# Kernel tuning notes

Measured on AMD Instinct MI355X. Metric: run time of the kernel, lower is better.

The kernel has to match this reference:

```python
import jax, jax.numpy as jnp
import numpy as np

D_MODEL = 1024
N_LAYER = 8
VOCAB = 32000
D_INNER = 2048
D_STATE = 16
DT_RANK = 64  # ceil(d_model/16)
KCONV = 4
SEQ = 2048


def causal_depthwise_conv(u, w):
    # u: [l, d_inner], w: [d_inner, 1, K]; causal padding (K-1, 0), groups=d_inner
    x = u.T[None]  # [1, d_inner, l]
    y = jax.lax.conv_general_dilated(
        x, w, window_strides=(1,), padding=[(KCONV - 1, 0)],
        dimension_numbers=("NCH", "OIH", "NCH"), feature_group_count=u.shape[1])
    return y[0].T  # [l, d_inner]


def selective_scan(u, dt, A, B, C, Dp):
    # u,dt: [l,d_in]; A: [d_in,n]; B,C: [l,n]; D: [d_in]; bilinear discretization
    dt_A = dt[:, :, None] * A[None, :, :]          # [l, d_in, n]
    dt_B = dt[:, :, None] * B[:, None, :]          # [l, d_in, n]
    denom = 1.0 - dt_A / 2
    dA = (1.0 + dt_A / 2) / denom
    dB = dt_B / denom

    def step(h, inp):
        ui, dAi, dBi, Ci = inp
        h = dAi * h + dBi * ui[:, None]            # [d_in, n]
        return h, h @ Ci                           # y_i: [d_in]

    h0 = jnp.zeros((u.shape[1], A.shape[1]), dtype=u.dtype)
    _, y = jax.lax.scan(step, h0, (u, dA, dB, C))
    return y + u * Dp


def mamba_layer(x, Wres, Win, Wconv, WB, WC, Wdt1, Wdt2, bdt, logA, Dp, Wout):
    # RMS pre-norm (no learned scale)
    xn = x * jax.lax.rsqrt(jnp.mean(x * x, axis=-1, keepdims=True) + 1e-6)
    res = xn @ Wres.T                              # [l, d_inner]
    u = xn @ Win.T                                 # [l, d_inner]
    u = causal_depthwise_conv(u, Wconv)
    u = jax.nn.silu(u)
    A = -jnp.exp(logA)                             # [d_inner, n]
    B = u @ WB.T                                   # [l, n]
    C = u @ WC.T                                   # [l, n]
    dt = jax.nn.softplus((u @ Wdt1.T) @ Wdt2.T + bdt)
    y = selective_scan(u, dt, A, B, C, Dp)
    y = y * jax.nn.silu(res)
    return x + y @ Wout.T                          # residual


def setup_inputs() -> dict:
    key = jax.random.key(0)
    ks = jax.random.split(key, 12)
    L = N_LAYER
    token_ids = jax.random.randint(ks[0], (SEQ,), 0, VOCAB)
    embed = jax.random.normal(ks[1], (VOCAB, D_MODEL), jnp.float32) * 0.02
    Wres = jax.random.normal(ks[2], (L, D_INNER, D_MODEL), jnp.float32) * 0.02
    Win = jax.random.normal(ks[3], (L, D_INNER, D_MODEL), jnp.float32) * 0.02
    Wconv = jax.random.normal(ks[4], (L, D_INNER, 1, KCONV), jnp.float32) * 0.3
    WB = jax.random.normal(ks[5], (L, D_STATE, D_INNER), jnp.float32) * 0.02
    WC = jax.random.normal(ks[6], (L, D_STATE, D_INNER), jnp.float32) * 0.02
    Wdt1 = jax.random.normal(ks[7], (L, DT_RANK, D_INNER), jnp.float32) / np.sqrt(D_INNER)
    Wdt2 = jax.random.uniform(ks[8], (L, D_INNER, DT_RANK), jnp.float32,
                              minval=-1 / np.sqrt(DT_RANK), maxval=1 / np.sqrt(DT_RANK))
    # inverse-softplus of dt ~ U[1e-3, 1e-1] in log space
    dt0 = jnp.exp(jax.random.uniform(ks[9], (L, D_INNER)) * (np.log(0.1) - np.log(0.001)) + np.log(0.001))
    bdt = dt0 + jnp.log(-jnp.expm1(-dt0))
    logA = jnp.log(jnp.broadcast_to(jnp.arange(1, D_STATE + 1, dtype=jnp.float32),
                                    (L, D_INNER, D_STATE)))
    Dp = jnp.ones((L, D_INNER), jnp.float32)
    Wout = jax.random.normal(ks[10], (L, D_MODEL, D_INNER), jnp.float32) * 0.02
    return dict(token_ids=token_ids, embed=embed, Wres=Wres, Win=Win, Wconv=Wconv,
                WB=WB, WC=WC, Wdt1=Wdt1, Wdt2=Wdt2, bdt=bdt, logA=logA, Dp=Dp, Wout=Wout)


def reference(token_ids, embed, Wres, Win, Wconv, WB, WC, Wdt1, Wdt2, bdt, logA, Dp, Wout):
    x = embed[token_ids]  # [l, d_model]
    for i in range(Wres.shape[0]):
        x = mamba_layer(x, Wres[i], Win[i], Wconv[i], WB[i], WC[i],
                        Wdt1[i], Wdt2[i], bdt[i], logA[i], Dp[i], Wout[i])
    return x @ embed.T  # [l, vocab] logits (tied embedding)
```

## Files before the change

kernel.cpp:

```cpp
#include <hip/hip_runtime.h>

#define SEQ 2048
#define DMODEL 1024
#define DINNER 2048
#define DSTATE 16
#define DTRANK 64
#define NLAYER 8
#define VOCAB 32000
#define NCHUNK 32
#define CLEN 64
#define PROJ_NCH 16
#define PROJ_KC 128

typedef float f32x4 __attribute__((ext_vector_type(4)));
typedef short bf16x8 __attribute__((ext_vector_type(8)));

__device__ __forceinline__ ushort f2bf(float f) {
  union { float f; unsigned u; } v; v.f = f;
  unsigned r = v.u + 0x7fffu + ((v.u >> 16) & 1u);
  return (ushort)(r >> 16);
}

__device__ __forceinline__ void lds_load16(const void* g, void* l) {
  __builtin_amdgcn_global_load_lds(
      (const __attribute__((address_space(1))) void*)g,
      (__attribute__((address_space(3))) void*)l, 16, 0, 0);
}

template<int BM, bool NTS>
__global__ __launch_bounds__(512, 2) void gemm8p_bt_bf16(
    const ushort* __restrict__ A, const ushort* __restrict__ B,
    float* __restrict__ C, int N, int K)
{
  constexpr int MFR = BM / 32;
  constexpr int MPP = MFR / 4;
  constexpr int ALOADS = BM / 128;
  __shared__ __align__(16) ushort As[2 * BM * 64];
  __shared__ __align__(16) ushort Bs[2 * 256 * 64];
  const int tid = threadIdx.x;
  const int lane = tid & 63;
  const int wid = tid >> 6;
  const int wr = wid >> 2, wc = wid & 3;
  const int rr = lane & 15, kq = lane >> 4;

  unsigned nwg = gridDim.x * gridDim.y;
  unsigned lb = blockIdx.y * gridDim.x + blockIdx.x;
  if ((nwg & 7u) == 0u) { unsigned cpx = nwg >> 3; lb = (lb & 7u) * cpx + (lb >> 3); }
  const int bm = (int)(lb % gridDim.x) * BM;
  const int bn = (int)(lb / gridDim.x) * 256;

  const ushort* Abase = A + (size_t)bm * K;
  const ushort* Bbase = B + (size_t)bn * K;

  auto stageA = [&](int buf, int h, int kt) {
    constexpr int HR = BM / 2;
#pragma unroll
    for (int L = 0; L < ALOADS; ++L) {
      int f = L * 512 + tid;
      int rl = f >> 3, g = f & 7;
      int gg = g ^ (rl & 7);
      lds_load16(Abase + (size_t)(h * HR + rl) * K + kt * 64 + gg * 8,
                 (void*)(As + buf * (BM * 64) + (h * HR + rl) * 64 + g * 8));
    }
  };
  auto stageB = [&](int buf, int h, int kt) {
#pragma unroll
    for (int L = 0; L < 2; ++L) {
      int f = L * 512 + tid;
      int rl = f >> 3, g = f & 7;
      int gg = g ^ (rl & 7);
      lds_load16(Bbase + (size_t)(h * 128 + rl) * K + kt * 64 + gg * 8,
                 (void*)(Bs + buf * (256 * 64) + (h * 128 + rl) * 64 + g * 8));
    }
  };
  auto rdA = [&](int buf, int r, int kbyte) {
    int sw = kbyte ^ ((r & 7) << 4);
    return *(const bf16x8*)(As + buf * (BM * 64) + r * 64 + (sw >> 1));
  };
  auto rdB = [&](int buf, int r, int kbyte) {
    int sw = kbyte ^ ((r & 7) << 4);
    return *(const bf16x8*)(Bs + buf * (256 * 64) + r * 64 + (sw >> 1));
  };

  f32x4 acc[MFR][4];
#pragma unroll
  for (int m = 0; m < MFR; ++m)
#pragma unroll
    for (int n = 0; n < 4; ++n) acc[m][n] = (f32x4){0.f, 0.f, 0.f, 0.f};

  const int NT = K >> 6;
  stageA(0, 0, 0); stageA(0, 1, 0); stageB(0, 0, 0); stageB(0, 1, 0);

  for (int t = 0; t < NT; ++t) {
    const int cur = t & 1;
    const bool more = (t + 1 < NT);
    if (more) stageA(cur ^ 1, 0, t + 1);
    if (more) {
      if constexpr (BM == 256) asm volatile("s_waitcnt vmcnt(2)" ::: "memory");
      else                     asm volatile("s_waitcnt vmcnt(1)" ::: "memory");
    } else {
      asm volatile("s_waitcnt vmcnt(0)" ::: "memory");
    }
    __syncthreads();

    bf16x8 bfr[4][2];
#pragma unroll
    for (int n = 0; n < 4; ++n)
#pragma unroll
      for (int kk = 0; kk < 2; ++kk)
        bfr[n][kk] = rdB(cur, wc * 64 + n * 16 + rr, kk * 64 + kq * 16);

#pragma unroll
    for (int mq = 0; mq < 4; ++mq) {
      if (mq == 1 && more) stageA(cur ^ 1, 1, t + 1);
      if (mq == 2 && more) stageB(cur ^ 1, 0, t + 1);
      if (mq == 3 && more) stageB(cur ^ 1, 1, t + 1);
      bf16x8 af[MPP][2];
#pragma unroll
      for (int mf = 0; mf < MPP; ++mf)
#pragma unroll
        for (int kk = 0; kk < 2; ++kk)
          af[mf][kk] = rdA(cur, wr * (BM / 2) + (mq * MPP + mf) * 16 + rr, kk * 64 + kq * 16);
      __builtin_amdgcn_s_setprio(1);
#pragma unroll
      for (int kk = 0; kk < 2; ++kk)
#pragma unroll
        for (int mf = 0; mf < MPP; ++mf)
#pragma unroll
          for (int n = 0; n < 4; ++n)
            acc[mq * MPP + mf][n] = __builtin_amdgcn_mfma_f32_16x16x32_bf16(
                af[mf][kk], bfr[n][kk], acc[mq * MPP + mf][n], 0, 0, 0);
      __builtin_amdgcn_s_setprio(0);
    }
    __syncthreads();
  }

  float* ep = (float*)Bs + wid * (16 * 68);
  const int cg = bn + wc * 64;
#pragma unroll
  for (int m = 0; m < MFR; ++m) {
    const int r0g = bm + wr * (BM / 2) + m * 16;
#pragma unroll
    for (int n = 0; n < 4; ++n)
#pragma unroll
      for (int j = 0; j < 4; ++j)
        ep[(kq * 4 + j) * 68 + n * 16 + rr] = acc[m][n][j];
#pragma unroll
    for (int i = 0; i < 4; ++i) {
      int row = i * 4 + kq;
      f32x4 v = *(const f32x4*)&ep[row * 68 + rr * 4];
      f32x4* dst = (f32x4*)&C[(size_t)(r0g + row) * N + cg + rr * 4];
      if constexpr (NTS) __builtin_nontemporal_store(v, dst);
      else *dst = v;
    }
  }
}

__global__ __launch_bounds__(256) void gemm_btk_bf16(
    const ushort* __restrict__ A, const ushort* __restrict__ B,
    float* __restrict__ Cp, int M, int N, int K)
{
  __shared__ __align__(16) ushort As[128 * 64];
  __shared__ __align__(16) ushort Bs[128 * 64];
  const int tid = threadIdx.x;
  const int lane = tid & 63;
  const int wave = tid >> 6;
  const int wr = wave >> 1, wc = wave & 1;
  const int KC = K >> 1;
  const int k0 = blockIdx.z * KC;

  unsigned nwg = gridDim.x * gridDim.y;
  unsigned lb = blockIdx.y * gridDim.x + blockIdx.x;
  if ((nwg & 7u) == 0u) {
    unsigned cpx = nwg >> 3;
    lb = (lb & 7u) * cpx + (lb >> 3);
  }
  const int bm = (lb % gridDim.x) * 128;
  const int bn = (lb / gridDim.x) * 128;
  const int rr = lane & 15, kq = lane >> 4;

  f32x4 acc[4][4];
#pragma unroll
  for (int m = 0; m < 4; ++m)
#pragma unroll
    for (int n = 0; n < 4; ++n) acc[m][n] = (f32x4){0.f, 0.f, 0.f, 0.f};

  for (int kt = 0; kt < KC; kt += 64) {
#pragma unroll
    for (int i = 0; i < 4; ++i) {
      int fb = i * 256 + tid;
      int row = fb >> 3, cb = fb & 7;
      lds_load16(A + (size_t)(bm + row) * K + k0 + kt + cb * 8, (void*)(As + (size_t)fb * 8));
      lds_load16(B + (size_t)(bn + row) * K + k0 + kt + cb * 8, (void*)(Bs + (size_t)fb * 8));
    }
    __syncthreads();
#pragma unroll
    for (int ks = 0; ks < 2; ++ks) {
      bf16x8 af[4], bfr[4];
      const int koff = ks * 32 + kq * 8;
#pragma unroll
      for (int m = 0; m < 4; ++m)
        af[m] = *(const bf16x8*)&As[(wr * 64 + m * 16 + rr) * 64 + koff];
#pragma unroll
      for (int n = 0; n < 4; ++n)
        bfr[n] = *(const bf16x8*)&Bs[(wc * 64 + n * 16 + rr) * 64 + koff];
#pragma unroll
      for (int m = 0; m < 4; ++m)
#pragma unroll
        for (int n = 0; n < 4; ++n)
          acc[m][n] = __builtin_amdgcn_mfma_f32_16x16x32_bf16(af[m], bfr[n], acc[m][n], 0, 0, 0);
    }
    __syncthreads();
  }
  float* C = Cp + (size_t)blockIdx.z * M * N;
#pragma unroll
  for (int m = 0; m < 4; ++m) {
    const int r0 = bm + wr * 64 + m * 16 + kq * 4;
#pragma unroll
    for (int n = 0; n < 4; ++n) {
      const int cc = bn + wc * 64 + n * 16 + rr;
#pragma unroll
      for (int j = 0; j < 4; ++j)
        C[(size_t)(r0 + j) * N + cc] = acc[m][n][j];
    }
  }
}

__global__ __launch_bounds__(256) void add3_kernel(
    const float* __restrict__ P0, const float* __restrict__ P1, float* __restrict__ x)
{
  size_t i = (size_t)blockIdx.x * 256 + threadIdx.x;
  float4 a = ((const float4*)P0)[i];
  float4 b = ((const float4*)P1)[i];
  float4 c = ((float4*)x)[i];
  c.x += a.x + b.x; c.y += a.y + b.y; c.z += a.z + b.z; c.w += a.w + b.w;
  ((float4*)x)[i] = c;
}

__global__ __launch_bounds__(256) void projgemm_f32(
    const float* __restrict__ A, const float* __restrict__ W,
    float* __restrict__ Cp, int M)
{
  __shared__ float As[64][65];
  __shared__ float Ws[96][65];
  const int t = threadIdx.x;
  const int bm = blockIdx.x * 64;
  const int kc = blockIdx.y * PROJ_KC;
  const int ty = t >> 4, tx = t & 15;
  const int r0 = ty * 4, c0 = tx * 6;
  float acc[4][6] = {};
  for (int kt = 0; kt < PROJ_KC; kt += 64) {
#pragma unroll
    for (int i = 0; i < 4; ++i) {
      int e4 = i * 256 + t;
      int r = e4 >> 4, c4 = (e4 & 15) * 4;
      *(float4*)&As[r][c4] = *(const float4*)&A[(size_t)(bm + r) * DINNER + kc + kt + c4];
    }
#pragma unroll
    for (int i = 0; i < 6; ++i) {
      int e4 = i * 256 + t;
      int r = e4 >> 4, c4 = (e4 & 15) * 4;
      *(float4*)&Ws[r][c4] = *(const float4*)&W[(size_t)r * DINNER + kc + kt + c4];
    }
    __syncthreads();
#pragma unroll 4
    for (int kk = 0; kk < 64; ++kk) {
      float a0 = As[r0][kk], a1 = As[r0 + 1][kk], a2 = As[r0 + 2][kk], a3 = As[r0 + 3][kk];
      float w0 = Ws[c0][kk], w1 = Ws[c0 + 1][kk], w2 = Ws[c0 + 2][kk];
      float w3 = Ws[c0 + 3][kk], w4 = Ws[c0 + 4][kk], w5 = Ws[c0 + 5][kk];
      acc[0][0] += a0 * w0; acc[0][1] += a0 * w1; acc[0][2] += a0 * w2;
      acc[0][3] += a0 * w3; acc[0][4] += a0 * w4; acc[0][5] += a0 * w5;
      acc[1][0] += a1 * w0; acc[1][1] += a1 * w1; acc[1][2] += a1 * w2;
      acc[1][3] += a1 * w3; acc[1][4] += a1 * w4; acc[1][5] += a1 * w5;
      acc[2][0] += a2 * w0; acc[2][1] += a2 * w1; acc[2][2] += a2 * w2;
      acc[2][3] += a2 * w3; acc[2][4] += a2 * w4; acc[2][5] += a2 * w5;
      acc[3][0] += a3 * w0; acc[3][1] += a3 * w1; acc[3][2] += a3 * w2;
      acc[3][3] += a3 * w3; acc[3][4] += a3 * w4; acc[3][5] += a3 * w5;
    }
    __syncthreads();
  }
  float* cp = Cp + (size_t)blockIdx.y * M * 96;
#pragma unroll
  for (int i = 0; i < 4; ++i)
#pragma unroll
    for (int j = 0; j < 6; ++j)
      cp[(size_t)(bm + r0 + i) * 96 + c0 + j] = acc[i][j];
}

__global__ __launch_bounds__(256) void proj_reduce(
    const float* __restrict__ Cp, float* __restrict__ bcdt, int M)
{
  int idx = blockIdx.x * 256 + threadIdx.x;
  float s = 0.f;
#pragma unroll
  for (int c = 0; c < PROJ_NCH; ++c) s += Cp[(size_t)c * M * 96 + idx];
  bcdt[idx] = s;
}

__global__ __launch_bounds__(256) void smallgemm_f32(
    const float* __restrict__ A, int lda,
    const float* __restrict__ W, int ldw,
    float* __restrict__ C, int ldc,
    const float* __restrict__ bias,
    int M, int N, int K, int act)
{
  __shared__ float As[64][65];
  __shared__ float Ws[64][65];
  const int t = threadIdx.x;
  const int bm = blockIdx.x * 64, bn = blockIdx.y * 64;
  const int r0 = (t >> 4) * 4;
  const int c0 = (t & 15) * 4;
  float acc[4][4] = {};

  for (int kt = 0; kt < K; kt += 64) {
#pragma unroll
    for (int i = 0; i < 16; ++i) {
      int idx = i * 256 + t;
      int r = idx >> 6, c = idx & 63;
      As[r][c] = A[(size_t)(bm + r) * lda + kt + c];
      int wrow = bn + r;
      Ws[r][c] = (wrow < N) ? W[(size_t)wrow * ldw + kt + c] : 0.f;
    }
    __syncthreads();
#pragma unroll 8
    for (int kk = 0; kk < 64; ++kk) {
      float a0 = As[r0][kk], a1 = As[r0 + 1][kk], a2 = As[r0 + 2][kk], a3 = As[r0 + 3][kk];
      float w0 = Ws[c0][kk], w1 = Ws[c0 + 1][kk], w2 = Ws[c0 + 2][kk], w3 = Ws[c0 + 3][kk];
      acc[0][0] += a0 * w0; acc[0][1] += a0 * w1; acc[0][2] += a0 * w2; acc[0][3] += a0 * w3;
      acc[1][0] += a1 * w0; acc[1][1] += a1 * w1; acc[1][2] += a1 * w2; acc[1][3] += a1 * w3;
      acc[2][0] += a2 * w0; acc[2][1] += a2 * w1; acc[2][2] += a2 * w2; acc[2][3] += a2 * w3;
      acc[3][0] += a3 * w0; acc[3][1] += a3 * w1; acc[3][2] += a3 * w2; acc[3][3] += a3 * w3;
    }
    __syncthreads();
  }
#pragma unroll
  for (int i = 0; i < 4; ++i)
#pragma unroll
    for (int j = 0; j < 4; ++j) {
      int cc = bn + c0 + j;
      if (cc < N) {
        float v = acc[i][j];
        if (bias) v += bias[cc];
        if (act == 1) v = (v > 20.f) ? v : log1pf(expf(v));
        C[(size_t)(bm + r0 + i) * ldc + cc] = v;
      }
    }
}

__global__ __launch_bounds__(256) void gather_kernel(
    const int* __restrict__ ids, const float* __restrict__ embed, float* __restrict__ x)
{
  int row = blockIdx.x;
  int id = ids[row];
  ((float4*)x)[(size_t)row * (DMODEL / 4) + threadIdx.x] =
      ((const float4*)(embed + (size_t)id * DMODEL))[threadIdx.x];
}

__global__ __launch_bounds__(256) void rmsnorm_kernel(
    const float* __restrict__ x, ushort* __restrict__ xnb)
{
  int row = blockIdx.x;
  float4 v = ((const float4*)(x + (size_t)row * DMODEL))[threadIdx.x];
  float s = v.x * v.x + v.y * v.y + v.z * v.z + v.w * v.w;
#pragma unroll
  for (int o = 32; o > 0; o >>= 1) s += __shfl_down(s, o);
  __shared__ float ws[4];
  if ((threadIdx.x & 63) == 0) ws[threadIdx.x >> 6] = s;
  __syncthreads();
  float tot = ws[0] + ws[1] + ws[2] + ws[3];
  float sc = rsqrtf(tot * (1.0f / DMODEL) + 1e-6f);
  ushort4 o4 = {f2bf(v.x * sc), f2bf(v.y * sc), f2bf(v.z * sc), f2bf(v.w * sc)};
  ((ushort4*)xnb)[(size_t)row * (DMODEL / 4) + threadIdx.x] = o4;
}

__global__ __launch_bounds__(256) void conv_silu_kernel(
    const float* __restrict__ u0, int ld, const float* __restrict__ Wconv,
    float* __restrict__ u)
{
  int idx = blockIdx.x * 256 + threadIdx.x;
  int d4 = idx & (DINNER / 4 - 1);
  int l = idx >> 9;
  int d0 = d4 * 4;
  float wt[4][4];
#pragma unroll
  for (int j = 0; j < 4; ++j) {
    float4 tv = *(const float4*)&Wconv[(d0 + j) * 4];
    wt[j][0] = tv.x; wt[j][1] = tv.y; wt[j][2] = tv.z; wt[j][3] = tv.w;
  }
  float a[4] = {0.f, 0.f, 0.f, 0.f};
#pragma unroll
  for (int k = 0; k < 4; ++k) {
    int ls = l - 3 + k;
    if (ls >= 0) {
      float4 uv = *(const float4*)&u0[(size_t)ls * ld + d0];
      a[0] += uv.x * wt[0][k];
      a[1] += uv.y * wt[1][k];
      a[2] += uv.z * wt[2][k];
      a[3] += uv.w * wt[3][k];
    }
  }
  float4 r;
  r.x = a[0] / (1.f + expf(-a[0]));
  r.y = a[1] / (1.f + expf(-a[1]));
  r.z = a[2] / (1.f + expf(-a[2]));
  r.w = a[3] / (1.f + expf(-a[3]));
  *(float4*)&u[(size_t)l * DINNER + d0] = r;
}

__global__ __launch_bounds__(256) void scan_pass1(
    const float* __restrict__ dt, const float* __restrict__ u,
    const float* __restrict__ bcdt, const float* __restrict__ logA,
    float* __restrict__ P, float* __restrict__ S)
{
  const int tid = threadIdx.x;
  const int n = tid & 15, dl = tid >> 4;
  const int dbase = blockIdx.x * 16;
  const int c = blockIdx.y;
  const int t0 = c * CLEN;
  const int d = dbase + dl;
  const float Aval = -expf(logA[d * DSTATE + n]);
  __shared__ float sdt[CLEN][16], su[CLEN][16], sB[CLEN][16];
  {
    int tt = tid >> 2, j0 = (tid & 3) * 4;
    *(float4*)&sdt[tt][j0] = *(const float4*)&dt[(size_t)(t0 + tt) * DINNER + dbase + j0];
    *(float4*)&su[tt][j0]  = *(const float4*)&u[(size_t)(t0 + tt) * DINNER + dbase + j0];
    *(float4*)&sB[tt][j0]  = *(const float4*)&bcdt[(size_t)(t0 + tt) * 96 + j0];
  }
  __syncthreads();
  float h = 0.f, pr = 1.f;
#pragma unroll 8
  for (int i = 0; i < CLEN; ++i) {
    float dtv = sdt[i][dl], uv = su[i][dl], Bv = sB[i][n];
    float dtA = dtv * Aval;
    float rinv = __builtin_amdgcn_rcpf(1.f - 0.5f * dtA);
    float dA = (1.f + 0.5f * dtA) * rinv;
    float dBu = dtv * Bv * rinv * uv;
    h = dA * h + dBu;
    pr *= dA;
  }
  size_t idx = (size_t)c * (DINNER * DSTATE) + (size_t)d * DSTATE + n;
  P[idx] = pr;
  S[idx] = h;
}

__global__ __launch_bounds__(256) void scan_pass2(
    const float* __restrict__ dt, const float* __restrict__ u,
    const float* __restrict__ bcdt, const float* __restrict__ logA,
    const float* __restrict__ Dp, const float* __restrict__ P,
    const float* __restrict__ S, const float* __restrict__ resu0,
    ushort* __restrict__ y2b)
{
  const int tid = threadIdx.x;
  const int n = tid & 15, dl = tid >> 4;
  const int dbase = blockIdx.x * 16;
  const int c = blockIdx.y;
  const int t0 = c * CLEN;
  const int d = dbase + dl;
  const float Aval = -expf(logA[d * DSTATE + n]);
  const float Dpv = Dp[d];
  __shared__ float sdt[CLEN][16], su[CLEN][16], sB[CLEN][16], sC[CLEN][16], sres[CLEN][16];
  {
    int tt = tid >> 2, j0 = (tid & 3) * 4;
    *(float4*)&sdt[tt][j0]  = *(const float4*)&dt[(size_t)(t0 + tt) * DINNER + dbase + j0];
    *(float4*)&su[tt][j0]   = *(const float4*)&u[(size_t)(t0 + tt) * DINNER + dbase + j0];
    *(float4*)&sB[tt][j0]   = *(const float4*)&bcdt[(size_t)(t0 + tt) * 96 + j0];
    *(float4*)&sC[tt][j0]   = *(const float4*)&bcdt[(size_t)(t0 + tt) * 96 + 16 + j0];
    *(float4*)&sres[tt][j0] = *(const float4*)&resu0[(size_t)(t0 + tt) * (2 * DINNER) + dbase + j0];
  }
  float h = 0.f;
  {
    const size_t base = (size_t)d * DSTATE + n;
#pragma unroll 4
    for (int cc = 0; cc < c; ++cc) {
      size_t o = (size_t)cc * (DINNER * DSTATE) + base;
      h = P[o] * h + S[o];
    }
  }
  __syncthreads();
#pragma unroll 4
  for (int i = 0; i < CLEN; ++i) {
    float dtv = sdt[i][dl], uv = su[i][dl];
    float dtA = dtv * Aval;
    float rinv = __builtin_amdgcn_rcpf(1.f - 0.5f * dtA);
    float dA = (1.f + 0.5f * dtA) * rinv;
    float dBu = dtv * sB[i][n] * rinv * uv;
    h = dA * h + dBu;
    float p = h * sC[i][n];
    p += __shfl_xor(p, 1);
    p += __shfl_xor(p, 2);
    p += __shfl_xor(p, 4);
    p += __shfl_xor(p, 8);
    if (n == 0) {
      float rv = sres[i][dl];
      float yv = (p + uv * Dpv) * (rv / (1.f + expf(-rv)));
      y2b[(size_t)(t0 + i) * DINNER + d] = f2bf(yv);
    }
  }
}

__global__ __launch_bounds__(256) void cast_bf16_kernel(
    const float* __restrict__ in, ushort* __restrict__ out, size_t n4)
{
  size_t i = (size_t)blockIdx.x * 256 + threadIdx.x;
  if (i >= n4) return;
  float4 v = ((const float4*)in)[i];
  ushort4 o = {f2bf(v.x), f2bf(v.y), f2bf(v.z), f2bf(v.w)};
  ((ushort4*)out)[i] = o;
}

__global__ __launch_bounds__(256) void cast_cat2_kernel(
    const float* __restrict__ Wres, const float* __restrict__ Win, ushort* __restrict__ out)
{
  size_t i4 = (size_t)blockIdx.x * 256 + threadIdx.x;
  size_t e0 = i4 * 4;
  int k = (int)(e0 & (DMODEL - 1));
  int r = (int)((e0 >> 10) & (2 * DINNER - 1));
  int l = (int)(e0 >> 22);
  const float* src = (r < DINNER)
      ? &Wres[(((size_t)l * DINNER + r) << 10) + k]
      : &Win[(((size_t)l * DINNER + (r - DINNER)) << 10) + k];
  float4 v = *(const float4*)src;
  ushort4 o = {f2bf(v.x), f2bf(v.y), f2bf(v.z), f2bf(v.w)};
  ((ushort4*)out)[i4] = o;
}

__global__ __launch_bounds__(256) void concat_wbcdt_kernel(
    const float* __restrict__ WB, const float* __restrict__ WC,
    const float* __restrict__ Wdt1, float* __restrict__ out)
{
  size_t idx = (size_t)blockIdx.x * 256 + threadIdx.x;
  int k = idx & (DINNER - 1);
  size_t rl = idx >> 11;
  int row = (int)(rl % 96);
  int l = (int)(rl / 96);
  float v;
  if (row < 16)       v = WB[((size_t)l * DSTATE + row) * DINNER + k];
  else if (row < 32)  v = WC[((size_t)l * DSTATE + (row - 16)) * DINNER + k];
  else                v = Wdt1[((size_t)l * DTRANK + (row - 32)) * DINNER + k];
  out[idx] = v;
}

extern "C" void kernel_launch(void* const* d_in, const int* in_sizes, int n_in,
                              void* d_out, int out_size, void* d_ws, size_t ws_size,
                              hipStream_t stream) {
  (void)in_sizes; (void)n_in; (void)out_size;
  const int* token_ids = (const int*)d_in[0];
  const float* embed = (const float*)d_in[1];
  const float* Wres = (const float*)d_in[2];
  const float* Win = (const float*)d_in[3];
  const float* Wconv = (const float*)d_in[4];
  const float* WB = (const float*)d_in[5];
  const float* WC = (const float*)d_in[6];
  const float* Wdt1 = (const float*)d_in[7];
  const float* Wdt2 = (const float*)d_in[8];
  const float* bdt = (const float*)d_in[9];
  const float* logA = (const float*)d_in[10];
  const float* Dp = (const float*)d_in[11];
  const float* Wout = (const float*)d_in[12];
  float* out = (float*)d_out;

  char* w = (char*)d_ws;
  auto alloc = [&](size_t bytes) {
    char* p = w;
    w += (bytes + 255) & ~(size_t)255;
    return p;
  };
  ushort* eb    = (ushort*)alloc((size_t)VOCAB * DMODEL * 2);
  ushort* wcatb = (ushort*)alloc((size_t)NLAYER * 2 * DINNER * DMODEL * 2);
  ushort* woutb = (ushort*)alloc((size_t)NLAYER * DMODEL * DINNER * 2);
  float* wbcdt  = (float*)alloc((size_t)NLAYER * 96 * DINNER * 4);
  float* x      = (float*)alloc((size_t)SEQ * DMODEL * 4);
  ushort* xnb   = (ushort*)alloc((size_t)SEQ * DMODEL * 2);
  float* resu0  = (float*)alloc((size_t)SEQ * 2 * DINNER * 4);
  float* u      = (float*)alloc((size_t)SEQ * DINNER * 4);
  float* bcdt   = (float*)alloc((size_t)SEQ * 96 * 4);
  float* dt     = (float*)alloc((size_t)SEQ * DINNER * 4);
  float* Cp     = (float*)alloc((size_t)PROJ_NCH * SEQ * 96 * 4);
  float* Cp2    = (float*)alloc((size_t)2 * SEQ * DMODEL * 4);
  float* Pbuf   = (float*)alloc((size_t)NCHUNK * DINNER * DSTATE * 4);
  float* Sbuf   = (float*)alloc((size_t)NCHUNK * DINNER * DSTATE * 4);
  ushort* y2b   = (ushort*)alloc((size_t)SEQ * DINNER * 2);
  ushort* xb    = (ushort*)alloc((size_t)SEQ * DMODEL * 2);
  if ((size_t)(w - (char*)d_ws) > ws_size) return;

  cast_bf16_kernel<<<VOCAB * DMODEL / 4 / 256, 256, 0, stream>>>(embed, eb, (size_t)VOCAB * DMODEL / 4);
  cast_cat2_kernel<<<NLAYER * 2 * DINNER * DMODEL / 4 / 256, 256, 0, stream>>>(Wres, Win, wcatb);
  cast_bf16_kernel<<<NLAYER * DMODEL * DINNER / 4 / 256, 256, 0, stream>>>(Wout, woutb, (size_t)NLAYER * DMODEL * DINNER / 4);
  concat_wbcdt_kernel<<<NLAYER * 96 * DINNER / 256, 256, 0, stream>>>(WB, WC, Wdt1, wbcdt);
  gather_kernel<<<SEQ, 256, 0, stream>>>(token_ids, embed, x);

  for (int i = 0; i < NLAYER; ++i) {
    const ushort* wcati = wcatb + (size_t)i * 2 * DINNER * DMODEL;
    const ushort* wouti = woutb + (size_t)i * DMODEL * DINNER;
    const float* wconvi = Wconv + (size_t)i * DINNER * 4;
    const float* wbcdti = wbcdt + (size_t)i * 96 * DINNER;
    const float* wdt2i = Wdt2 + (size_t)i * DINNER * DTRANK;
    const float* bdti = bdt + (size_t)i * DINNER;
    const float* logAi = logA + (size_t)i * DINNER * DSTATE;
    const float* Dpi = Dp + (size_t)i * DINNER;

    rmsnorm_kernel<<<SEQ, 256, 0, stream>>>(x, xnb);
    gemm8p_bt_bf16<128, false><<<dim3(SEQ / 128, 2 * DINNER / 256), 512, 0, stream>>>(
        xnb, wcati, resu0, 2 * DINNER, DMODEL);
    conv_silu_kernel<<<SEQ * DINNER / 4 / 256, 256, 0, stream>>>(resu0 + DINNER, 2 * DINNER, wconvi, u);
    projgemm_f32<<<dim3(SEQ / 64, PROJ_NCH), 256, 0, stream>>>(u, wbcdti, Cp, SEQ);
    proj_reduce<<<SEQ * 96 / 256, 256, 0, stream>>>(Cp, bcdt, SEQ);
    smallgemm_f32<<<dim3(SEQ / 64, DINNER / 64), 256, 0, stream>>>(
        bcdt + 32, 96, wdt2i, DTRANK, dt, DINNER, bdti, SEQ, DINNER, DTRANK, 1);
    dim3 gs(DINNER / 16, NCHUNK);
    scan_pass1<<<gs, 256, 0, stream>>>(dt, u, bcdt, logAi, Pbuf, Sbuf);
    scan_pass2<<<gs, 256, 0, stream>>>(dt, u, bcdt, logAi, Dpi, Pbuf, Sbuf, resu0, y2b);
    gemm_btk_bf16<<<dim3(SEQ / 128, DMODEL / 128, 2), 256, 0, stream>>>(
        y2b, wouti, Cp2, SEQ, DMODEL, DINNER);
    add3_kernel<<<SEQ * DMODEL / 4 / 256, 256, 0, stream>>>(
        Cp2, Cp2 + (size_t)SEQ * DMODEL, x);
  }
  cast_bf16_kernel<<<SEQ * DMODEL / 4 / 256, 256, 0, stream>>>(x, xb, (size_t)SEQ * DMODEL / 4);
  gemm8p_bt_bf16<256, true><<<dim3(SEQ / 256, VOCAB / 256), 512, 0, stream>>>(
      xb, eb, out, VOCAB, DMODEL);
}
```

Before: 2.308 ms.

## Replace 8-wave GEMM with 128x128 4-wave kernel and fuse RMSnorm into residual add

Swaps the 512-thread GEMM, which used 128/256x256 tiles and staggered staging, for a simpler 256-thread 128x128 tile kernel. That kernel stages A and B together into double-buffered LDS. RMS normalization and the bf16 cast are folded into the gather and residual-add kernels, which removes the separate rmsnorm and final cast launches. The smaller tiles mean more workgroups and less staggered load overlap, with more global traffic per flop for the large vocab GEMM.

```diff
diff --git a/kernel.cpp b/kernel.cpp
--- a/kernel.cpp
+++ b/kernel.cpp
@@ -27,119 +27,93 @@
       (__attribute__((address_space(3))) void*)l, 16, 0, 0);
 }
 
-template<int BM, bool NTS>
-__global__ __launch_bounds__(512, 2) void gemm8p_bt_bf16(
+template<bool NTS>
+__global__ __launch_bounds__(256, 2) void gemm2p_bt_bf16(
     const ushort* __restrict__ A, const ushort* __restrict__ B,
     float* __restrict__ C, int N, int K)
 {
-  constexpr int MFR = BM / 32;
-  constexpr int MPP = MFR / 4;
-  constexpr int ALOADS = BM / 128;
-  __shared__ __align__(16) ushort As[2 * BM * 64];
-  __shared__ __align__(16) ushort Bs[2 * 256 * 64];
+  __shared__ __align__(16) ushort As[2 * 128 * 64];
+  __shared__ __align__(16) ushort Bs[2 * 128 * 64];
   const int tid = threadIdx.x;
   const int lane = tid & 63;
-  const int wid = tid >> 6;
-  const int wr = wid >> 2, wc = wid & 3;
+  const int wave = tid >> 6;
+  const int wr = wave >> 1, wc = wave & 1;
   const int rr = lane & 15, kq = lane >> 4;
 
   unsigned nwg = gridDim.x * gridDim.y;
   unsigned lb = blockIdx.y * gridDim.x + blockIdx.x;
   if ((nwg & 7u) == 0u) { unsigned cpx = nwg >> 3; lb = (lb & 7u) * cpx + (lb >> 3); }
-  const int bm = (int)(lb % gridDim.x) * BM;
-  const int bn = (int)(lb / gridDim.x) * 256;
+  const int bm = (int)(lb % gridDim.x) * 128;
+  const int bn = (int)(lb / gridDim.x) * 128;
 
   const ushort* Abase = A + (size_t)bm * K;
   const ushort* Bbase = B + (size_t)bn * K;
 
-  auto stageA = [&](int buf, int h, int kt) {
-    constexpr int HR = BM / 2;
-#pragma unroll
-    for (int L = 0; L < ALOADS; ++L) {
-      int f = L * 512 + tid;
+  auto stage = [&](int buf, int kt) {
+#pragma unroll
+    for (int i = 0; i < 4; ++i) {
+      int f = i * 256 + tid;
       int rl = f >> 3, g = f & 7;
       int gg = g ^ (rl & 7);
-      lds_load16(Abase + (size_t)(h * HR + rl) * K + kt * 64 + gg * 8,
-                 (void*)(As + buf * (BM * 64) + (h * HR + rl) * 64 + g * 8));
-    }
-  };
-  auto stageB = [&](int buf, int h, int kt) {
-#pragma unroll
-    for (int L = 0; L < 2; ++L) {
-      int f = L * 512 + tid;
-      int rl = f >> 3, g = f & 7;
-      int gg = g ^ (rl & 7);
-      lds_load16(Bbase + (size_t)(h * 128 + rl) * K + kt * 64 + gg * 8,
-                 (void*)(Bs + buf * (256 * 64) + (h * 128 + rl) * 64 + g * 8));
+      lds_load16(Abase + (size_t)rl * K + kt * 64 + gg * 8,
+                 (void*)(As + buf * 8192 + rl * 64 + g * 8));
+      lds_load16(Bbase + (size_t)rl * K + kt * 64 + gg * 8,
+                 (void*)(Bs + buf * 8192 + rl * 64 + g * 8));
     }
   };
   auto rdA = [&](int buf, int r, int kbyte) {
     int sw = kbyte ^ ((r & 7) << 4);
-    return *(const bf16x8*)(As + buf * (BM * 64) + r * 64 + (sw >> 1));
+    return *(const bf16x8*)(As + buf * 8192 + r * 64 + (sw >> 1));
   };
   auto rdB = [&](int buf, int r, int kbyte) {
     int sw = kbyte ^ ((r & 7) << 4);
-    return *(const bf16x8*)(Bs + buf * (256 * 64) + r * 64 + (sw >> 1));
+    return *(const bf16x8*)(Bs + buf * 8192 + r * 64 + (sw >> 1));
   };
 
-  f32x4 acc[MFR][4];
-#pragma unroll
-  for (int m = 0; m < MFR; ++m)
+  f32x4 acc[4][4];
+#pragma unroll
+  for (int m = 0; m < 4; ++m)
 #pragma unroll
     for (int n = 0; n < 4; ++n) acc[m][n] = (f32x4){0.f, 0.f, 0.f, 0.f};
 
   const int NT = K >> 6;
-  stageA(0, 0, 0); stageA(0, 1, 0); stageB(0, 0, 0); stageB(0, 1, 0);
+  stage(0, 0);
 
   for (int t = 0; t < NT; ++t) {
     const int cur = t & 1;
-    const bool more = (t + 1 < NT);
-    if (more) stageA(cur ^ 1, 0, t + 1);
-    if (more) {
-      if constexpr (BM == 256) asm volatile("s_waitcnt vmcnt(2)" ::: "memory");
-      else                     asm volatile("s_waitcnt vmcnt(1)" ::: "memory");
+    if (t + 1 < NT) {
+      stage(cur ^ 1, t + 1);
+      asm volatile("s_waitcnt vmcnt(8)" ::: "memory");
     } else {
       asm volatile("s_waitcnt vmcnt(0)" ::: "memory");
     }
     __syncthreads();
-
-    bf16x8 bfr[4][2];
-#pragma unroll
-    for (int n = 0; n < 4; ++n)
-#pragma unroll
-      for (int kk = 0; kk < 2; ++kk)
-        bfr[n][kk] = rdB(cur, wc * 64 + n * 16 + rr, kk * 64 + kq * 16);
-
-#pragma unroll
-    for (int mq = 0; mq < 4; ++mq) {
-      if (mq == 1 && more) stageA(cur ^ 1, 1, t + 1);
-      if (mq == 2 && more) stageB(cur ^ 1, 0, t + 1);
-      if (mq == 3 && more) stageB(cur ^ 1, 1, t + 1);
-      bf16x8 af[MPP][2];
-#pragma unroll
-      for (int mf = 0; mf < MPP; ++mf)
-#pragma unroll
-        for (int kk = 0; kk < 2; ++kk)
-          af[mf][kk] = rdA(cur, wr * (BM / 2) + (mq * MPP + mf) * 16 + rr, kk * 64 + kq * 16);
+#pragma unroll
+    for (int ks = 0; ks < 2; ++ks) {
+      const int kbyte = ks * 64 + kq * 16;
+      bf16x8 af[4], bfr[4];
+#pragma unroll
+      for (int m = 0; m < 4; ++m)
+        af[m] = rdA(cur, wr * 64 + m * 16 + rr, kbyte);
+#pragma unroll
+      for (int n = 0; n < 4; ++n)
+        bfr[n] = rdB(cur, wc * 64 + n * 16 + rr, kbyte);
       __builtin_amdgcn_s_setprio(1);
 #pragma unroll
-      for (int kk = 0; kk < 2; ++kk)
-#pragma unroll
-        for (int mf = 0; mf < MPP; ++mf)
-#pragma unroll
-          for (int n = 0; n < 4; ++n)
-            acc[mq * MPP + mf][n] = __builtin_amdgcn_mfma_f32_16x16x32_bf16(
-                af[mf][kk], bfr[n][kk], acc[mq * MPP + mf][n], 0, 0, 0);
+      for (int m = 0; m < 4; ++m)
+#pragma unroll
+        for (int n = 0; n < 4; ++n)
+          acc[m][n] = __builtin_amdgcn_mfma_f32_16x16x32_bf16(af[m], bfr[n], acc[m][n], 0, 0, 0);
       __builtin_amdgcn_s_setprio(0);
     }
     __syncthreads();
   }
 
-  float* ep = (float*)Bs + wid * (16 * 68);
+  float* ep = (float*)Bs + wave * (16 * 68);
   const int cg = bn + wc * 64;
 #pragma unroll
-  for (int m = 0; m < MFR; ++m) {
-    const int r0g = bm + wr * (BM / 2) + m * 16;
+  for (int m = 0; m < 4; ++m) {
+    const int r0g = bm + wr * 64 + m * 16;
 #pragma unroll
     for (int n = 0; n < 4; ++n)
 #pragma unroll
@@ -226,15 +200,50 @@
   }
 }
 
-__global__ __launch_bounds__(256) void add3_kernel(
-    const float* __restrict__ P0, const float* __restrict__ P1, float* __restrict__ x)
-{
-  size_t i = (size_t)blockIdx.x * 256 + threadIdx.x;
-  float4 a = ((const float4*)P0)[i];
-  float4 b = ((const float4*)P1)[i];
-  float4 c = ((float4*)x)[i];
+__global__ __launch_bounds__(256) void add3_rms_kernel(
+    const float* __restrict__ P0, const float* __restrict__ P1,
+    float* __restrict__ x, ushort* __restrict__ dst, int donorm)
+{
+  size_t o = (size_t)blockIdx.x * (DMODEL / 4) + threadIdx.x;
+  float4 a = ((const float4*)P0)[o];
+  float4 b = ((const float4*)P1)[o];
+  float4 c = ((float4*)x)[o];
   c.x += a.x + b.x; c.y += a.y + b.y; c.z += a.z + b.z; c.w += a.w + b.w;
-  ((float4*)x)[i] = c;
+  ((float4*)x)[o] = c;
+  float sc = 1.f;
+  if (donorm) {
+    float s = c.x * c.x + c.y * c.y + c.z * c.z + c.w * c.w;
+#pragma unroll
+    for (int off = 32; off > 0; off >>= 1) s += __shfl_down(s, off);
+    __shared__ float ws[4];
+    if ((threadIdx.x & 63) == 0) ws[threadIdx.x >> 6] = s;
+    __syncthreads();
+    float tot = ws[0] + ws[1] + ws[2] + ws[3];
+    sc = rsqrtf(tot * (1.0f / DMODEL) + 1e-6f);
+  }
+  ushort4 o4 = {f2bf(c.x * sc), f2bf(c.y * sc), f2bf(c.z * sc), f2bf(c.w * sc)};
+  ((ushort4*)dst)[o] = o4;
+}
+
+__global__ __launch_bounds__(256) void gather_rms_kernel(
+    const int* __restrict__ ids, const float* __restrict__ embed,
+    float* __restrict__ x, ushort* __restrict__ xnb)
+{
+  int row = blockIdx.x;
+  int id = ids[row];
+  float4 v = ((const float4*)(embed + (size_t)id * DMODEL))[threadIdx.x];
+  size_t o = (size_t)row * (DMODEL / 4) + threadIdx.x;
+  ((float4*)x)[o] = v;
+  float s = v.x * v.x + v.y * v.y + v.z * v.z + v.w * v.w;
+#pragma unroll
+  for (int off = 32; off > 0; off >>= 1) s += __shfl_down(s, off);
+  __shared__ float ws[4];
+  if ((threadIdx.x & 63) == 0) ws[threadIdx.x >> 6] = s;
+  __syncthreads();
+  float tot = ws[0] + ws[1] + ws[2] + ws[3];
+  float sc = rsqrtf(tot * (1.0f / DMODEL) + 1e-6f);
+  ushort4 o4 = {f2bf(v.x * sc), f2bf(v.y * sc), f2bf(v.z * sc), f2bf(v.w * sc)};
+  ((ushort4*)xnb)[o] = o4;
 }
 
 __global__ __launch_bounds__(256) void projgemm_f32(
@@ -345,32 +354,6 @@
         C[(size_t)(bm + r0 + i) * ldc + cc] = v;
       }
     }
-}
-
-__global__ __launch_bounds__(256) void gather_kernel(
-    const int* __restrict__ ids, const float* __restrict__ embed, float* __restrict__ x)
-{
-  int row = blockIdx.x;
-  int id = ids[row];
-  ((float4*)x)[(size_t)row * (DMODEL / 4) + threadIdx.x] =
-      ((const float4*)(embed + (size_t)id * DMODEL))[threadIdx.x];
-}
-
-__global__ __launch_bounds__(256) void rmsnorm_kernel(
-    const float* __restrict__ x, ushort* __restrict__ xnb)
-{
-  int row = blockIdx.x;
-  float4 v = ((const float4*)(x + (size_t)row * DMODEL))[threadIdx.x];
-  float s = v.x * v.x + v.y * v.y + v.z * v.z + v.w * v.w;
-#pragma unroll
-  for (int o = 32; o > 0; o >>= 1) s += __shfl_down(s, o);
-  __shared__ float ws[4];
-  if ((threadIdx.x & 63) == 0) ws[threadIdx.x >> 6] = s;
-  __syncthreads();
-  float tot = ws[0] + ws[1] + ws[2] + ws[3];
-  float sc = rsqrtf(tot * (1.0f / DMODEL) + 1e-6f);
-  ushort4 o4 = {f2bf(v.x * sc), f2bf(v.y * sc), f2bf(v.z * sc), f2bf(v.w * sc)};
-  ((ushort4*)xnb)[(size_t)row * (DMODEL / 4) + threadIdx.x] = o4;
 }
 
 __global__ __launch_bounds__(256) void conv_silu_kernel(
@@ -587,7 +570,7 @@
   cast_cat2_kernel<<<NLAYER * 2 * DINNER * DMODEL / 4 / 256, 256, 0, stream>>>(Wres, Win, wcatb);
   cast_bf16_kernel<<<NLAYER * DMODEL * DINNER / 4 / 256, 256, 0, stream>>>(Wout, woutb, (size_t)NLAYER * DMODEL * DINNER / 4);
   concat_wbcdt_kernel<<<NLAYER * 96 * DINNER / 256, 256, 0, stream>>>(WB, WC, Wdt1, wbcdt);
-  gather_kernel<<<SEQ, 256, 0, stream>>>(token_ids, embed, x);
+  gather_rms_kernel<<<SEQ, 256, 0, stream>>>(token_ids, embed, x, xnb);
 
   for (int i = 0; i < NLAYER; ++i) {
     const ushort* wcati = wcatb + (size_t)i * 2 * DINNER * DMODEL;
@@ -599,8 +582,7 @@
     const float* logAi = logA + (size_t)i * DINNER * DSTATE;
     const float* Dpi = Dp + (size_t)i * DINNER;
 
-    rmsnorm_kernel<<<SEQ, 256, 0, stream>>>(x, xnb);
-    gemm8p_bt_bf16<128, false><<<dim3(SEQ / 128, 2 * DINNER / 256), 512, 0, stream>>>(
+    gemm2p_bt_bf16<false><<<dim3(SEQ / 128, 2 * DINNER / 128), 256, 0, stream>>>(
         xnb, wcati, resu0, 2 * DINNER, DMODEL);
     conv_silu_kernel<<<SEQ * DINNER / 4 / 256, 256, 0, stream>>>(resu0 + DINNER, 2 * DINNER, wconvi, u);
     projgemm_f32<<<dim3(SEQ / 64, PROJ_NCH), 256, 0, stream>>>(u, wbcdti, Cp, SEQ);
@@ -612,10 +594,10 @@
     scan_pass2<<<gs, 256, 0, stream>>>(dt, u, bcdt, logAi, Dpi, Pbuf, Sbuf, resu0, y2b);
     gemm_btk_bf16<<<dim3(SEQ / 128, DMODEL / 128, 2), 256, 0, stream>>>(
         y2b, wouti, Cp2, SEQ, DMODEL, DINNER);
-    add3_kernel<<<SEQ * DMODEL / 4 / 256, 256, 0, stream>>>(
-        Cp2, Cp2 + (size_t)SEQ * DMODEL, x);
-  }
-  cast_bf16_kernel<<<SEQ * DMODEL / 4 / 256, 256, 0, stream>>>(x, xb, (size_t)SEQ * DMODEL / 4);
-  gemm8p_bt_bf16<256, true><<<dim3(SEQ / 256, VOCAB / 256), 512, 0, stream>>>(
+    add3_rms_kernel<<<SEQ, 256, 0, stream>>>(
+        Cp2, Cp2 + (size_t)SEQ * DMODEL, x,
+        (i < NLAYER - 1) ? xnb : xb, (i < NLAYER - 1) ? 1 : 0);
+  }
+  gemm2p_bt_bf16<true><<<dim3(SEQ / 128, VOCAB / 128), 256, 0, stream>>>(
       xb, eb, out, VOCAB, DMODEL);
 }
```

After: 2.268 ms. Within noise of the previous version (-1.7%).
